# Performance work log

Measured on AMD Instinct MI355X. Metric: run time of the kernel, lower is better.

The kernel has to match this reference:

```python
import jax, jax.numpy as jnp
import numpy as np

BS, NQ, NCLS = 16, 128, 3
T, P = 480, 72          # total targets, points per curve
COST_CLASS_W = 1.0
CURVES_W = 1.0
LOWER_W = 1.0
UPPER_W = 1.0


def setup_inputs() -> dict:
    key = jax.random.key(0)
    k1, k2, k3, k4, k5, k6, k7 = jax.random.split(key, 7)
    pred_logits = jax.random.normal(k1, (BS, NQ, NCLS), dtype=jnp.float32)
    pred_curves = jax.random.uniform(k2, (BS, NQ, 8), dtype=jnp.float32)
    # targets: [T, 5 + 2P] = [class_id, lower_y, upper_y, lower_x, upper_x, xs(P), ys(P)]
    ids = jax.random.randint(k3, (T,), 0, NCLS).astype(jnp.float32)
    ends = jax.random.uniform(k4, (T, 4), dtype=jnp.float32)  # ly, uy, lx, ux
    xs = jax.random.uniform(k5, (T, P), dtype=jnp.float32)
    ys = jax.random.uniform(k6, (T, P), dtype=jnp.float32)
    # variable number of valid points per lane; invalid points marked x = -1
    counts = jax.random.randint(k7, (T,), P // 2, P + 1)
    valid = jnp.arange(P)[None, :] < counts[:, None]
    xs = jnp.where(valid, xs, -1.0)
    targets = jnp.concatenate([ids[:, None], ends, xs, ys], axis=1)
    return {"pred_logits": pred_logits, "pred_curves": pred_curves, "targets": targets}


def reference(pred_logits, pred_curves, targets):
    bs, nq, _ = pred_logits.shape
    BN = bs * nq
    out_prob = jax.nn.softmax(pred_logits.reshape(BN, -1), axis=-1)
    tgt_ids = targets[:, 0].astype(jnp.int32)
    cost_class = -out_prob[:, tgt_ids]                      # [BN, T]

    ob = pred_curves.reshape(BN, 8)
    ly, uy, lx, ux = targets[:, 1], targets[:, 2], targets[:, 3], targets[:, 4]
    # L1 cdist on scalars == abs diff; averaged over (y, x) endpoint coords
    cost_lower = 0.5 * (jnp.abs(ob[:, 0:1] - ly[None, :]) + jnp.abs(ob[:, 2:3] - lx[None, :]))
    cost_upper = 0.5 * (jnp.abs(ob[:, 1:2] - uy[None, :]) + jnp.abs(ob[:, 3:4] - ux[None, :]))

    p = (targets.shape[1] - 5) // 2
    txs = targets[:, 5:5 + p]                               # [T, P]
    tys = targets[:, 5 + p:]                                # [T, P]
    valid = txs >= 0                                        # [T, P]
    per = jnp.sum(valid, axis=1).astype(jnp.float32)        # [T]
    total = jnp.sum(valid).astype(jnp.float32)
    w = jnp.sqrt(total / per)
    w = w / jnp.max(w)                                      # [T]

    p1 = jnp.stack([lx, ly], axis=-1)                       # [T, 2]
    p2 = jnp.stack([ux, uy], axis=-1)
    d = p2 - p1                                             # [T, 2]
    pi = jnp.stack([txs, tys], axis=-1)                     # [T, P, 2]
    p1pi = pi - p1[:, None, :]
    dot = jnp.einsum('tk,tpk->tp', d, p1pi)                 # [T, P]
    nrm = jnp.sqrt(jnp.sum(d * d, axis=-1))                 # [T]
    # original: proj = dot / nrm, then lam = proj / nrm
    lam = (dot / nrm[:, None]) / nrm[:, None]               # [T, P]

    a3, a2 = ob[:, 4], ob[:, 5]
    a1 = ob[:, 3] - a3 - a2 - ob[:, 2]
    a0 = ob[:, 2]
    b3, b2 = ob[:, 6], ob[:, 7]
    b1 = ob[:, 1] - b3 - b2 - ob[:, 0]
    b0 = ob[:, 0]

    L = lam[:, :, None]                                     # [T, P, 1] broadcast vs [BN]
    L2 = L * L
    L3 = L2 * L
    ox = a3 * L3 + a2 * L2 + a1 * L + a0                    # [T, P, BN]
    oy = b3 * L3 + b2 * L2 + b1 * L + b0

    diff = (txs[:, :, None] - ox) ** 2 + (tys[:, :, None] - oy) ** 2
    cost_polys = jnp.sum(jnp.where(valid[:, :, None], diff, 0.0), axis=1)  # [T, BN]
    cost_polys = cost_polys.T * w[None, :]                  # [BN, T]

    C = (COST_CLASS_W * cost_class + CURVES_W * cost_polys / 10.0
         + LOWER_W * cost_lower + UPPER_W * cost_upper)
    return C.reshape(bs, nq, -1)
```

## Files before the change

kernel.cpp:

```cpp
#include <hip/hip_runtime.h>
#include <math.h>

#define BS   16
#define NQ   128
#define NCLS 3
#define T    480
#define P    72
#define BN   (BS * NQ)
#define TROW (5 + 2 * P)
#define BNB  4

#define MD_OFF_B 0
#define EF_OFF_B 61440
#define BD_OFF_B 72960
#define BF_OFF_B 204032

__global__ __launch_bounds__(64) void moments_kernel(const float* __restrict__ targets,
                                                     double* __restrict__ MD,
                                                     float* __restrict__ EF) {
    int t    = blockIdx.x;
    int lane = threadIdx.x;
    const float* row = targets + (size_t)t * TROW;
    float ly = row[1], uy = row[2], lx = row[3], ux = row[4];
    float dx = ux - lx, dy = uy - ly;
    float nrm = sqrtf(dx * dx + dy * dy);

    double v[17];
#pragma unroll
    for (int i = 0; i < 17; ++i) v[i] = 0.0;

    for (int p = lane; p < P; p += 64) {
        float tx = row[5 + p];
        float ty = row[5 + P + p];
        if (tx >= 0.0f) {
            float lamf = dx * (tx - lx) + dy * (ty - ly);
            lamf = lamf / nrm / nrm;
            double L   = (double)lamf;
            double txd = (double)tx, tyd = (double)ty;
            double lp = 1.0;
#pragma unroll
            for (int j = 0; j < 7; ++j) {
                v[j] += lp;
                if (j < 4) {
                    v[7 + j]  += txd * lp;
                    v[11 + j] += tyd * lp;
                }
                lp *= L;
            }
            v[15] += txd * txd + tyd * tyd;
            v[16] += 1.0;
        }
    }

#pragma unroll
    for (int off = 32; off > 0; off >>= 1) {
#pragma unroll
        for (int i = 0; i < 17; ++i) v[i] += __shfl_down(v[i], off);
    }

    if (lane == 0) {
#pragma unroll
        for (int j = 0; j < 7; ++j) MD[j * T + t] = v[j];
#pragma unroll
        for (int k = 0; k < 4; ++k) {
            MD[(7 + k) * T + t]  = -2.0 * v[7 + k];
            MD[(11 + k) * T + t] = -2.0 * v[11 + k];
        }
        MD[15 * T + t] = v[15];
        EF[0 * T + t] = ly;
        EF[1 * T + t] = uy;
        EF[2 * T + t] = lx;
        EF[3 * T + t] = ux;
        EF[4 * T + t] = (float)v[16];
        EF[5 * T + t] = row[0];
    }
}

__global__ __launch_bounds__(256) void bnprep_kernel(const float* __restrict__ logits,
                                                     const float* __restrict__ curves,
                                                     double* __restrict__ BD,
                                                     float* __restrict__ BF) {
    int bn = blockIdx.x * 256 + threadIdx.x;
    const float* ob = curves + (size_t)bn * 8;
    float o0 = ob[0], o1 = ob[1], o2 = ob[2], o3 = ob[3];
    float o4 = ob[4], o5 = ob[5], o6 = ob[6], o7 = ob[7];
    float a0 = o2, a1 = o3 - o4 - o5 - o2, a2 = o5, a3 = o4;
    float b0 = o0, b1 = o1 - o6 - o7 - o0, b2 = o7, b3 = o6;

    double A0 = a0, A1 = a1, A2 = a2, A3 = a3;
    double B0 = b0, B1 = b1, B2 = b2, B3 = b3;
    double* Pd = BD + (size_t)bn * 8;
    Pd[0] = A0 * A0 + B0 * B0;
    Pd[1] = 2.0 * (A0 * A1 + B0 * B1);
    Pd[2] = 2.0 * (A0 * A2 + B0 * B2) + A1 * A1 + B1 * B1;
    Pd[3] = 2.0 * (A0 * A3 + A1 * A2 + B0 * B3 + B1 * B2);
    Pd[4] = 2.0 * (A1 * A3 + B1 * B3) + A2 * A2 + B2 * B2;
    Pd[5] = 2.0 * (A2 * A3 + B2 * B3);
    Pd[6] = A3 * A3 + B3 * B3;
    Pd[7] = 0.0;

    const float* lg = logits + (size_t)bn * NCLS;
    float l0 = lg[0], l1 = lg[1], l2 = lg[2];
    float mx = fmaxf(l0, fmaxf(l1, l2));
    float e0 = expf(l0 - mx), e1 = expf(l1 - mx), e2 = expf(l2 - mx);
    float inv = 1.0f / (e0 + e1 + e2);

    float* fb = BF + (size_t)bn * 16;
    fb[0] = a0; fb[1] = a1; fb[2] = a2; fb[3] = a3;
    fb[4] = b0; fb[5] = b1; fb[6] = b2; fb[7] = b3;
    fb[8] = o1; fb[9] = o3;
    fb[10] = e0 * inv; fb[11] = e1 * inv; fb[12] = e2 * inv;
    fb[13] = 0.0f; fb[14] = 0.0f; fb[15] = 0.0f;
}

__global__ __launch_bounds__(512) void cost_kernel(const double* __restrict__ MD,
                                                   const float* __restrict__ EF,
                                                   const double* __restrict__ BD,
                                                   const float* __restrict__ BF,
                                                   float* __restrict__ out) {
    __shared__ float smin[512];
    int t   = threadIdx.x;
    int bn0 = blockIdx.x * BNB;

    float per = (t < T) ? EF[4 * T + t] : 1e30f;
    smin[t] = per;
    __syncthreads();
    for (int s = 256; s > 0; s >>= 1) {
        if (t < s) smin[t] = fminf(smin[t], smin[t + s]);
        __syncthreads();
    }
    float per_min = smin[0];

    if (t >= T) return;
    float w = sqrtf(per_min / per);

    double m[16];
#pragma unroll
    for (int r = 0; r < 16; ++r) m[r] = MD[r * T + t];
    float ly = EF[0 * T + t], uy = EF[1 * T + t];
    float lx = EF[2 * T + t], ux = EF[3 * T + t];
    int   id = (int)EF[5 * T + t];

#pragma unroll
    for (int j = 0; j < BNB; ++j) {
        const double* Pd = BD + (size_t)(bn0 + j) * 8;
        const float*  fb = BF + (size_t)(bn0 + j) * 16;
        double acc = m[15];
        acc += Pd[0] * m[0] + Pd[1] * m[1] + Pd[2] * m[2] + Pd[3] * m[3]
             + Pd[4] * m[4] + Pd[5] * m[5] + Pd[6] * m[6];
        acc += (double)fb[0] * m[7]  + (double)fb[1] * m[8]
             + (double)fb[2] * m[9]  + (double)fb[3] * m[10];
        acc += (double)fb[4] * m[11] + (double)fb[5] * m[12]
             + (double)fb[6] * m[13] + (double)fb[7] * m[14];
        float cp = (float)acc * w * 0.1f;
        float cl = 0.5f * (fabsf(fb[4] - ly) + fabsf(fb[0] - lx));
        float cu = 0.5f * (fabsf(fb[8] - uy) + fabsf(fb[9] - ux));
        float prob = (id == 0) ? fb[10] : ((id == 1) ? fb[11] : fb[12]);
        out[(size_t)(bn0 + j) * T + t] = -prob + cp + cl + cu;
    }
}

extern "C" void kernel_launch(void* const* d_in, const int* in_sizes, int n_in,
                              void* d_out, int out_size, void* d_ws, size_t ws_size,
                              hipStream_t stream) {
    const float* logits  = (const float*)d_in[0];
    const float* curves  = (const float*)d_in[1];
    const float* targets = (const float*)d_in[2];
    float* out = (float*)d_out;
    char*  ws  = (char*)d_ws;

    double* MD = (double*)(ws + MD_OFF_B);
    float*  EF = (float*) (ws + EF_OFF_B);
    double* BD = (double*)(ws + BD_OFF_B);
    float*  BF = (float*) (ws + BF_OFF_B);

    moments_kernel<<<T, 64, 0, stream>>>(targets, MD, EF);
    bnprep_kernel<<<BN / 256, 256, 0, stream>>>(logits, curves, BD, BF);
    cost_kernel<<<BN / BNB, 512, 0, stream>>>(MD, EF, BD, BF, out);
}
```

Before: 69.54 us.

## Fuse per-query prep into cost kernel and use shuffle-based min reduction

Removes the separate bnprep kernel and has each cost-kernel thread recompute the polynomial coefficient products and softmax for its query directly from the raw inputs. This drops one kernel launch and the global round trip through the BD/BF workspace. The cost is redundant double-precision arithmetic and exp per thread, repeated across all 480 targets. The block min reduction over point counts also moves from a shared-memory tree with many barriers to wave shuffles plus a single barrier.

```diff
diff --git a/kernel.cpp b/kernel.cpp
--- a/kernel.cpp
+++ b/kernel.cpp
@@ -12,8 +12,6 @@
 
 #define MD_OFF_B 0
 #define EF_OFF_B 61440
-#define BD_OFF_B 72960
-#define BF_OFF_B 204032
 
 __global__ __launch_bounds__(64) void moments_kernel(const float* __restrict__ targets,
                                                      double* __restrict__ MD,
@@ -76,60 +74,26 @@
     }
 }
 
-__global__ __launch_bounds__(256) void bnprep_kernel(const float* __restrict__ logits,
-                                                     const float* __restrict__ curves,
-                                                     double* __restrict__ BD,
-                                                     float* __restrict__ BF) {
-    int bn = blockIdx.x * 256 + threadIdx.x;
-    const float* ob = curves + (size_t)bn * 8;
-    float o0 = ob[0], o1 = ob[1], o2 = ob[2], o3 = ob[3];
-    float o4 = ob[4], o5 = ob[5], o6 = ob[6], o7 = ob[7];
-    float a0 = o2, a1 = o3 - o4 - o5 - o2, a2 = o5, a3 = o4;
-    float b0 = o0, b1 = o1 - o6 - o7 - o0, b2 = o7, b3 = o6;
-
-    double A0 = a0, A1 = a1, A2 = a2, A3 = a3;
-    double B0 = b0, B1 = b1, B2 = b2, B3 = b3;
-    double* Pd = BD + (size_t)bn * 8;
-    Pd[0] = A0 * A0 + B0 * B0;
-    Pd[1] = 2.0 * (A0 * A1 + B0 * B1);
-    Pd[2] = 2.0 * (A0 * A2 + B0 * B2) + A1 * A1 + B1 * B1;
-    Pd[3] = 2.0 * (A0 * A3 + A1 * A2 + B0 * B3 + B1 * B2);
-    Pd[4] = 2.0 * (A1 * A3 + B1 * B3) + A2 * A2 + B2 * B2;
-    Pd[5] = 2.0 * (A2 * A3 + B2 * B3);
-    Pd[6] = A3 * A3 + B3 * B3;
-    Pd[7] = 0.0;
-
-    const float* lg = logits + (size_t)bn * NCLS;
-    float l0 = lg[0], l1 = lg[1], l2 = lg[2];
-    float mx = fmaxf(l0, fmaxf(l1, l2));
-    float e0 = expf(l0 - mx), e1 = expf(l1 - mx), e2 = expf(l2 - mx);
-    float inv = 1.0f / (e0 + e1 + e2);
-
-    float* fb = BF + (size_t)bn * 16;
-    fb[0] = a0; fb[1] = a1; fb[2] = a2; fb[3] = a3;
-    fb[4] = b0; fb[5] = b1; fb[6] = b2; fb[7] = b3;
-    fb[8] = o1; fb[9] = o3;
-    fb[10] = e0 * inv; fb[11] = e1 * inv; fb[12] = e2 * inv;
-    fb[13] = 0.0f; fb[14] = 0.0f; fb[15] = 0.0f;
-}
-
-__global__ __launch_bounds__(512) void cost_kernel(const double* __restrict__ MD,
+__global__ __launch_bounds__(512) void cost_kernel(const float* __restrict__ logits,
+                                                   const float* __restrict__ curves,
+                                                   const double* __restrict__ MD,
                                                    const float* __restrict__ EF,
-                                                   const double* __restrict__ BD,
-                                                   const float* __restrict__ BF,
                                                    float* __restrict__ out) {
-    __shared__ float smin[512];
-    int t   = threadIdx.x;
-    int bn0 = blockIdx.x * BNB;
+    __shared__ float wavemin[8];
+    int t    = threadIdx.x;
+    int bn0  = blockIdx.x * BNB;
+    int lane = t & 63;
+    int wid  = t >> 6;
 
     float per = (t < T) ? EF[4 * T + t] : 1e30f;
-    smin[t] = per;
+    float pm = per;
+#pragma unroll
+    for (int off = 32; off > 0; off >>= 1) pm = fminf(pm, __shfl_xor(pm, off));
+    if (lane == 0) wavemin[wid] = pm;
     __syncthreads();
-    for (int s = 256; s > 0; s >>= 1) {
-        if (t < s) smin[t] = fminf(smin[t], smin[t + s]);
-        __syncthreads();
-    }
-    float per_min = smin[0];
+    float per_min = wavemin[0];
+#pragma unroll
+    for (int i = 1; i < 8; ++i) per_min = fminf(per_min, wavemin[i]);
 
     if (t >= T) return;
     float w = sqrtf(per_min / per);
@@ -143,20 +107,37 @@
 
 #pragma unroll
     for (int j = 0; j < BNB; ++j) {
-        const double* Pd = BD + (size_t)(bn0 + j) * 8;
-        const float*  fb = BF + (size_t)(bn0 + j) * 16;
-        double acc = m[15];
-        acc += Pd[0] * m[0] + Pd[1] * m[1] + Pd[2] * m[2] + Pd[3] * m[3]
-             + Pd[4] * m[4] + Pd[5] * m[5] + Pd[6] * m[6];
-        acc += (double)fb[0] * m[7]  + (double)fb[1] * m[8]
-             + (double)fb[2] * m[9]  + (double)fb[3] * m[10];
-        acc += (double)fb[4] * m[11] + (double)fb[5] * m[12]
-             + (double)fb[6] * m[13] + (double)fb[7] * m[14];
+        int bn = bn0 + j;
+        const float* ob = curves + (size_t)bn * 8;
+        float o0 = ob[0], o1 = ob[1], o2 = ob[2], o3 = ob[3];
+        float o4 = ob[4], o5 = ob[5], o6 = ob[6], o7 = ob[7];
+        float a0 = o2, a1 = o3 - o4 - o5 - o2, a2 = o5, a3 = o4;
+        float b0 = o0, b1 = o1 - o6 - o7 - o0, b2 = o7, b3 = o6;
+
+        double A0 = a0, A1 = a1, A2 = a2, A3 = a3;
+        double B0 = b0, B1 = b1, B2 = b2, B3 = b3;
+        double acc = m[15]
+            + (A0 * A0 + B0 * B0) * m[0]
+            + 2.0 * (A0 * A1 + B0 * B1) * m[1]
+            + (2.0 * (A0 * A2 + B0 * B2) + A1 * A1 + B1 * B1) * m[2]
+            + 2.0 * (A0 * A3 + A1 * A2 + B0 * B3 + B1 * B2) * m[3]
+            + (2.0 * (A1 * A3 + B1 * B3) + A2 * A2 + B2 * B2) * m[4]
+            + 2.0 * (A2 * A3 + B2 * B3) * m[5]
+            + (A3 * A3 + B3 * B3) * m[6]
+            + A0 * m[7]  + A1 * m[8]  + A2 * m[9]  + A3 * m[10]
+            + B0 * m[11] + B1 * m[12] + B2 * m[13] + B3 * m[14];
+
+        const float* lg = logits + (size_t)bn * NCLS;
+        float l0 = lg[0], l1 = lg[1], l2 = lg[2];
+        float mx = fmaxf(l0, fmaxf(l1, l2));
+        float e0 = __expf(l0 - mx), e1 = __expf(l1 - mx), e2 = __expf(l2 - mx);
+        float inv = 1.0f / (e0 + e1 + e2);
+        float prob = (id == 0) ? e0 * inv : ((id == 1) ? e1 * inv : e2 * inv);
+
         float cp = (float)acc * w * 0.1f;
-        float cl = 0.5f * (fabsf(fb[4] - ly) + fabsf(fb[0] - lx));
-        float cu = 0.5f * (fabsf(fb[8] - uy) + fabsf(fb[9] - ux));
-        float prob = (id == 0) ? fb[10] : ((id == 1) ? fb[11] : fb[12]);
-        out[(size_t)(bn0 + j) * T + t] = -prob + cp + cl + cu;
+        float cl = 0.5f * (fabsf(b0 - ly) + fabsf(a0 - lx));
+        float cu = 0.5f * (fabsf(o1 - uy) + fabsf(o3 - ux));
+        out[(size_t)bn * T + t] = -prob + cp + cl + cu;
     }
 }
 
@@ -171,10 +152,7 @@
 
     double* MD = (double*)(ws + MD_OFF_B);
     float*  EF = (float*) (ws + EF_OFF_B);
-    double* BD = (double*)(ws + BD_OFF_B);
-    float*  BF = (float*) (ws + BF_OFF_B);
 
     moments_kernel<<<T, 64, 0, stream>>>(targets, MD, EF);
-    bnprep_kernel<<<BN / 256, 256, 0, stream>>>(logits, curves, BD, BF);
-    cost_kernel<<<BN / BNB, 512, 0, stream>>>(MD, EF, BD, BF, out);
+    cost_kernel<<<BN / BNB, 512, 0, stream>>>(logits, curves, MD, EF, out);
 }
```

Measured after the change: 66.84 us, median of 2. 1.04x faster.
